# Kernel optimization log

Measured on AMD Instinct MI355X. Metric: run time of the kernel, lower is better.

The kernel has to match this reference:

```python
import jax, jax.numpy as jnp
import numpy as np

EPS = 1e-5

def _sparse_conv(x, nbr, W):
    # x: [N, Cin], nbr: [N, K] indices into rows of x, W: [K, Cin, Cout]
    # Minkowski-style kernel-map conv: gather neighbor feats, contract per offset.
    return jnp.einsum('nkc,kcd->nd', x[nbr], W)

def _bn(x, gamma, beta):
    # BatchNorm over all points (training-mode, biased variance)
    mu = x.mean(axis=0)
    var = x.var(axis=0)
    return (x - mu) * jax.lax.rsqrt(var + EPS) * gamma + beta

def setup_inputs() -> dict:
    key = jax.random.key(0)
    ks = jax.random.split(key, 6)
    N, K, Cin, Cout = 100000, 27, 64, 128
    x = jax.random.normal(ks[0], (N, Cin), dtype=jnp.float32)
    nbr = jax.random.randint(ks[1], (N, K), 0, N, dtype=jnp.int64)
    W1 = jax.random.normal(ks[2], (K, Cin, Cout), dtype=jnp.float32) / np.sqrt(K * Cin)
    W2 = jax.random.normal(ks[3], (K, Cout, Cout), dtype=jnp.float32) / np.sqrt(K * Cout)
    Wd = jax.random.normal(ks[4], (Cin, Cout), dtype=jnp.float32) / np.sqrt(Cin)
    ones = jnp.ones((Cout,), jnp.float32)
    zeros = jnp.zeros((Cout,), jnp.float32)
    return {"x": x, "nbr": nbr, "W1": W1, "g1": ones, "b1": zeros,
            "W2": W2, "g2": ones, "b2": zeros, "Wd": Wd, "gd": ones, "bd": zeros}

def reference(x, nbr, W1, g1, b1, W2, g2, b2, Wd, gd, bd):
    h = jax.nn.relu(_bn(_sparse_conv(x, nbr, W1), g1, b1))
    h = jax.nn.relu(_bn(_sparse_conv(h, nbr, W2), g2, b2))
    # downsample branch (input_nc != output_nc): 1x1 sparse conv == matmul, + BN
    res = _bn(x @ Wd, gd, bd)
    return h + res
```

## Files before the change

kernel.cpp:

```cpp
#include <hip/hip_runtime.h>
#include <hip/hip_bf16.h>

typedef unsigned short u16;
typedef unsigned int   u32;

#define COUT 128
#define KNB  27

typedef __attribute__((ext_vector_type(8))) __bf16 bf16x8;
typedef __attribute__((ext_vector_type(4))) float  f32x4;

__device__ float g_sum[2][128], g_sq[2][128];
__device__ float g_colsum[64], g_G[4096];
__device__ float g_sc[3][128], g_sh[3][128];
__device__ int   g_f32;
__device__ int   g_i64;
__device__ __attribute__((aligned(16))) u16 g_W1t[KNB * 128 * 64];
__device__ __attribute__((aligned(16))) u16 g_W2t[KNB * 128 * 128];

__device__ __forceinline__ float b2f(u32 u) {
    union { float f; u32 i; } v; v.i = u << 16; return v.f;
}
__device__ __forceinline__ u16 f2b(float f) {
    union { float f; u32 i; } v; v.f = f;
    u32 r = v.i + 0x7fffu + ((v.i >> 16) & 1u);
    return (u16)(r >> 16);
}
__device__ __forceinline__ float ldf(const void* p, int i, bool f32) {
    return f32 ? ((const float*)p)[i] : b2f((u32)((const u16*)p)[i]);
}

__device__ __forceinline__ void gld16(const void* g, void* l) {
    __builtin_amdgcn_global_load_lds(
        (const __attribute__((address_space(1))) u32*)g,
        (__attribute__((address_space(3))) u32*)l, 16, 0, 0);
}

__device__ __forceinline__ void lds_sync() {
    asm volatile("s_waitcnt lgkmcnt(0)" ::: "memory");
    __builtin_amdgcn_s_barrier();
    asm volatile("" ::: "memory");
}

__global__ void probe_zero_kernel(const u16* __restrict__ g1w, const int* __restrict__ nbr)
{
    int t = threadIdx.x;
    if (t == 0) {
        g_f32 = (g1w[0] == 0) ? 1 : 0;
        g_i64 = ((nbr[1] | nbr[3] | nbr[5] | nbr[7]) == 0) ? 1 : 0;
    }
    for (int i = t; i < 128; i += 256) {
        g_sum[0][i] = 0.f; g_sq[0][i] = 0.f;
        g_sum[1][i] = 0.f; g_sq[1][i] = 0.f;
    }
    for (int i = t; i < 64; i += 256) g_colsum[i] = 0.f;
    for (int i = t; i < 4096; i += 256) g_G[i] = 0.f;
}

__global__ void convert_w_kernel(const void* __restrict__ W1, const void* __restrict__ W2,
                                 const void* __restrict__ x, u16* __restrict__ xb, int N)
{
    const bool f32 = (g_f32 != 0);
    const int total1 = KNB * 64 * 128;
    const int total2 = KNB * 128 * 128;
    const int stride = gridDim.x * 256;
    for (int e = blockIdx.x * 256 + threadIdx.x; e < total1 + total2; e += stride) {
        if (e < total1) {
            int k = e / (64 * 128), r = e % (64 * 128);
            int c = r / 128, d = r % 128;
            g_W1t[(k * 128 + d) * 64 + c] = f2b(ldf(W1, e, f32));
        } else {
            int e2 = e - total1;
            int k = e2 / (128 * 128), r = e2 % (128 * 128);
            int c = r / 128, d = r % 128;
            g_W2t[(k * 128 + d) * 128 + c] = f2b(ldf(W2, e2, f32));
        }
    }
    const int totalx4 = (N * 64) / 4;
    for (int e = blockIdx.x * 256 + threadIdx.x; e < totalx4; e += stride) {
        if (f32) {
            float4 v = ((const float4*)x)[e];
            ushort4 r;
            r.x = f2b(v.x); r.y = f2b(v.y); r.z = f2b(v.z); r.w = f2b(v.w);
            ((ushort4*)xb)[e] = r;
        } else {
            ((uint2*)xb)[e] = ((const uint2*)x)[e];
        }
    }
}

__global__ __launch_bounds__(256)
void bn_relu_kernel(u16* __restrict__ tmp, int N)
{
    const int t  = threadIdx.x;
    const int c0 = (t & 15) * 8;
    float sc[8], sh[8];
#pragma unroll
    for (int j = 0; j < 8; ++j) { sc[j] = g_sc[0][c0 + j]; sh[j] = g_sh[0][c0 + j]; }
    const int total = N * (COUT / 8);
    for (int e = blockIdx.x * 256 + t; e < total; e += gridDim.x * 256) {
        uint4 u = ((const uint4*)tmp)[e];
        float v[8] = { b2f(u.x & 0xffffu), b2f(u.x >> 16),
                       b2f(u.y & 0xffffu), b2f(u.y >> 16),
                       b2f(u.z & 0xffffu), b2f(u.z >> 16),
                       b2f(u.w & 0xffffu), b2f(u.w >> 16) };
#pragma unroll
        for (int j = 0; j < 8; ++j) v[j] = fmaxf(fmaf(v[j], sc[j], sh[j]), 0.f);
        uint4 o;
        o.x = (u32)f2b(v[0]) | ((u32)f2b(v[1]) << 16);
        o.y = (u32)f2b(v[2]) | ((u32)f2b(v[3]) << 16);
        o.z = (u32)f2b(v[4]) | ((u32)f2b(v[5]) << 16);
        o.w = (u32)f2b(v[6]) | ((u32)f2b(v[7]) << 16);
        ((uint4*)tmp)[e] = o;
    }
}

template<int CIN, bool OUTF32, int WSEL, int SSEL>
__global__ __launch_bounds__(256, 2)
void spconv_mfma(const u16* __restrict__ src, const int* __restrict__ nbr,
                 void* __restrict__ outv, int N)
{
    constexpr int CHUNKS  = CIN / 64;
    constexpr int STEPS   = KNB * CHUNKS;
    constexpr int MAINEND = STEPS & ~1;
    const u16* __restrict__ Wt = (WSEL == 1) ? g_W1t : g_W2t;

    __shared__ __attribute__((aligned(16))) u16 As[2 * 8192];
    __shared__ __attribute__((aligned(16))) u16 Bs[2 * 8192];
    __shared__ u32 nbrl[128 * 28];

    const int t    = threadIdx.x;
    const int lane = t & 63;
    const int w    = t >> 6;
    const int mh   = lane & 15;
    const int qh   = lane >> 4;
    const int wm   = w >> 1;
    const int wn   = w & 1;
    const int n0   = blockIdx.x * 128;
    const int kst  = (g_i64 != 0) ? 2 : 1;

    const int r8   = lane >> 3;
    const int gaw  = ((lane & 7) ^ (r8 & 7)) * 8;

    for (int e = t; e < 128 * KNB; e += 256) {
        int row = e / KNB, kk = e - row * KNB;
        int gr  = n0 + row;
        int grc = (gr < N) ? gr : (N - 1);
        nbrl[row * 28 + kk] = (u32)nbr[(size_t)grc * (KNB * kst) + (size_t)kk * kst];
    }
    __syncthreads();

    int aoff[2][4];
#pragma unroll
    for (int mt = 0; mt < 4; ++mt) {
        int rr   = wm * 64 + mt * 16 + mh;
        int base = (rr >> 3) * 512 + (rr & 7) * 64;
        aoff[0][mt] = base + ((qh       ^ (mh & 7)) * 8);
        aoff[1][mt] = base + (((4 + qh) ^ (mh & 7)) * 8);
    }

    f32x4 acc[4][4];
#pragma unroll
    for (int a = 0; a < 4; ++a)
#pragma unroll
        for (int b = 0; b < 4; ++b) acc[a][b] = (f32x4){0.f, 0.f, 0.f, 0.f};

    int idx0[4], idxE[4], idxO[4];

#define KOF(S)  ((CHUNKS == 2) ? ((S) >> 1) : (S))
#define CB(S)   ((CHUNKS == 2) ? (((S) & 1) * 64) : 0)

#define IDXRD(DST, S) do { \
    int kk_ = KOF(S); if (kk_ > KNB - 1) kk_ = KNB - 1; \
    _Pragma("unroll") \
    for (int j_ = 0; j_ < 4; ++j_) \
        DST[j_] = (int)nbrl[(w * 32 + j_ * 8 + r8) * 28 + kk_]; \
} while (0)

#define ISSUE_STEP(BUFO, IDX, S) do { \
    const int cb_ = CB(S); const int k_ = KOF(S); \
    _Pragma("unroll") \
    for (int j_ = 0; j_ < 4; ++j_) { \
        u32 r_ = (u32)(IDX)[j_]; if (r_ >= (u32)N) r_ = 0; \
        gld16(src + (size_t)r_ * CIN + cb_ + gaw, \
              &As[(BUFO) + (w * 4 + j_) * 512]); \
    } \
    _Pragma("unroll") \
    for (int j_ = 0; j_ < 4; ++j_) { \
        const int sx_ = w * 4 + j_;                     \
        gld16(Wt + ((size_t)k_ * 128 + (sx_ >> 1) * 16 + mh) * CIN + cb_ \
                 + (sx_ & 1) * 32 + qh * 8, \
              &Bs[(BUFO) + sx_ * 512]); \
    } \
} while (0)

#define MFMA_PHASE(BUFO) do { \
    __builtin_amdgcn_s_setprio(1); \
    _Pragma("unroll") \
    for (int ks_ = 0; ks_ < 2; ++ks_) { \
        bf16x8 af_[4]; \
        _Pragma("unroll") \
        for (int mt_ = 0; mt_ < 4; ++mt_) \
            af_[mt_] = *(const bf16x8*)&As[(BUFO) + aoff[ks_][mt_]]; \
        _Pragma("unroll") \
        for (int nt_ = 0; nt_ < 4; ++nt_) { \
            bf16x8 bf_ = *(const bf16x8*)&Bs[(BUFO) + \
                (((wn * 4 + nt_) * 2 + ks_) * 512) + lane * 8]; \
            _Pragma("unroll") \
            for (int mt_ = 0; mt_ < 4; ++mt_) \
                acc[mt_][nt_] = __builtin_amdgcn_mfma_f32_16x16x32_bf16( \
                    af_[mt_], bf_, acc[mt_][nt_], 0, 0, 0); \
        } \
    } \
    __builtin_amdgcn_s_setprio(0); \
} while (0)

    IDXRD(idx0, 0);
    IDXRD(idxO, 1);
    ISSUE_STEP(0, idx0, 0);
    IDXRD(idxE, 2);

#pragma clang loop unroll(disable)
    for (int s = 0; s < MAINEND; s += 2) {
        lds_sync();
        ISSUE_STEP(8192, idxO, s + 1);
        IDXRD(idxO, s + 3);
        asm volatile("s_waitcnt vmcnt(8)" ::: "memory");
        __builtin_amdgcn_s_barrier();
        asm volatile("" ::: "memory");
        MFMA_PHASE(0);

        lds_sync();
        if (s + 2 < STEPS) {
            ISSUE_STEP(0, idxE, s + 2);
            IDXRD(idxE, s + 4);
            asm volatile("s_waitcnt vmcnt(8)" ::: "memory");
        } else {
            asm volatile("s_waitcnt vmcnt(0)" ::: "memory");
        }
        __builtin_amdgcn_s_barrier();
        asm volatile("" ::: "memory");
        MFMA_PHASE(8192);
    }
    if constexpr (STEPS & 1) {
        lds_sync();
        asm volatile("s_waitcnt vmcnt(0)" ::: "memory");
        __builtin_amdgcn_s_barrier();
        asm volatile("" ::: "memory");
        MFMA_PHASE(0);
    }

#pragma unroll
    for (int mt = 0; mt < 4; ++mt) {
#pragma unroll
        for (int r4 = 0; r4 < 4; ++r4) {
            int gr = n0 + (wm * 4 + mt) * 16 + qh * 4 + r4;
            if (gr < N) {
#pragma unroll
                for (int nt = 0; nt < 4; ++nt) {
                    float val = acc[mt][nt][r4];
                    size_t off = (size_t)gr * COUT + (wn * 4 + nt) * 16 + mh;
                    if constexpr (OUTF32) ((float*)outv)[off] = val;
                    else                  ((u16*)outv)[off]   = f2b(val);
                }
            }
        }
    }

    if constexpr (SSEL >= 0) {
        float sS[4], sQ[4];
#pragma unroll
        for (int nt = 0; nt < 4; ++nt) { sS[nt] = 0.f; sQ[nt] = 0.f; }
#pragma unroll
        for (int mt = 0; mt < 4; ++mt) {
#pragma unroll
            for (int r4 = 0; r4 < 4; ++r4) {
                int gr = n0 + (wm * 4 + mt) * 16 + qh * 4 + r4;
                bool ok = (gr < N);
#pragma unroll
                for (int nt = 0; nt < 4; ++nt) {
                    float v = ok ? acc[mt][nt][r4] : 0.f;
                    sS[nt] += v;
                    sQ[nt] = fmaf(v, v, sQ[nt]);
                }
            }
        }
#pragma unroll
        for (int nt = 0; nt < 4; ++nt) {
            sS[nt] += __shfl_xor(sS[nt], 16);
            sS[nt] += __shfl_xor(sS[nt], 32);
            sQ[nt] += __shfl_xor(sQ[nt], 16);
            sQ[nt] += __shfl_xor(sQ[nt], 32);
        }
        lds_sync();
        float* red = (float*)As;
        if (lane < 16) {
#pragma unroll
            for (int nt = 0; nt < 4; ++nt) {
                red[w * 64 + nt * 16 + lane]       = sS[nt];
                red[256 + w * 64 + nt * 16 + lane] = sQ[nt];
            }
        }
        lds_sync();
        if (t < 128) {
            int hi = t >> 6, lo = t & 63;
            float S = red[hi * 64 + lo] + red[(hi + 2) * 64 + lo];
            float Q = red[256 + hi * 64 + lo] + red[256 + (hi + 2) * 64 + lo];
            atomicAdd(&g_sum[SSEL][t], S);
            atomicAdd(&g_sq[SSEL][t],  Q);
        }
    }
#undef KOF
#undef CB
#undef IDXRD
#undef ISSUE_STEP
#undef MFMA_PHASE
}

template<int SEL>
__global__ void finalize_kernel(const void* __restrict__ g, const void* __restrict__ b,
                                float invN)
{
    const bool f32 = (g_f32 != 0);
    int c = threadIdx.x;
    float mu  = g_sum[SEL][c] * invN;
    float var = fmaxf(g_sq[SEL][c] * invN - mu * mu, 0.f);
    float rs  = rsqrtf(var + 1e-5f);
    float sc  = rs * ldf(g, c, f32);
    g_sc[SEL][c] = sc;
    g_sh[SEL][c] = ldf(b, c, f32) - mu * sc;
}

__global__ __launch_bounds__(256)
void xstats_kernel(const void* __restrict__ xv, int N)
{
    __shared__ float xs[16 * 64];
    const bool f32 = (g_f32 != 0);
    const int t  = threadIdx.x;
    const int c  = t >> 2;
    const int cb = (t & 3) * 16;
    float acc[16];
#pragma unroll
    for (int j = 0; j < 16; ++j) acc[j] = 0.f;
    float cs = 0.f;

    for (int r0 = blockIdx.x * 16; r0 < N; r0 += gridDim.x * 16) {
        __syncthreads();
        {
            int e = t * 4;
            int rr = e >> 6, qq = e & 63;
            int row = r0 + rr;
            size_t off = (size_t)min(row, N - 1) * 64 + qq;
            bool ok = (row < N);
            float v0, v1, v2, v3;
            if (f32) {
                float4 vv = *(const float4*)((const float*)xv + off);
                v0 = vv.x; v1 = vv.y; v2 = vv.z; v3 = vv.w;
            } else {
                uint2 u = *(const uint2*)((const u16*)xv + off);
                v0 = b2f(u.x & 0xffffu); v1 = b2f(u.x >> 16);
                v2 = b2f(u.y & 0xffffu); v3 = b2f(u.y >> 16);
            }
            xs[e + 0] = ok ? v0 : 0.f;
            xs[e + 1] = ok ? v1 : 0.f;
            xs[e + 2] = ok ? v2 : 0.f;
            xs[e + 3] = ok ? v3 : 0.f;
        }
        __syncthreads();
#pragma unroll
        for (int rr = 0; rr < 16; ++rr) {
            float a = xs[rr * 64 + c];
#pragma unroll
            for (int j = 0; j < 16; ++j)
                acc[j] = fmaf(a, xs[rr * 64 + cb + j], acc[j]);
        }
        if (t < 64) {
#pragma unroll
            for (int rr = 0; rr < 16; ++rr) cs += xs[rr * 64 + t];
        }
    }
#pragma unroll
    for (int j = 0; j < 16; ++j) atomicAdd(&g_G[c * 64 + cb + j], acc[j]);
    if (t < 64) atomicAdd(&g_colsum[t], cs);
}

__global__ __launch_bounds__(128)
void finalize_d_kernel(const void* __restrict__ Wd, const void* __restrict__ gd,
                       const void* __restrict__ bd, float invN)
{
    __shared__ float Gs[64 * 64];
    const bool f32 = (g_f32 != 0);
    const int t = threadIdx.x;
    for (int e = t; e < 4096; e += 128) Gs[e] = g_G[e];
    __syncthreads();
    float w[64];
#pragma unroll
    for (int c = 0; c < 64; ++c) w[c] = ldf(Wd, c * 128 + t, f32);
    float s = 0.f, q = 0.f;
    for (int c = 0; c < 64; ++c) {
        float inner = 0.f;
#pragma unroll 8
        for (int cc = 0; cc < 64; ++cc) inner = fmaf(Gs[c * 64 + cc], w[cc], inner);
        q = fmaf(w[c], inner, q);
        s = fmaf(g_colsum[c], w[c], s);
    }
    float mu  = s * invN;
    float var = fmaxf(q * invN - mu * mu, 0.f);
    float rs  = rsqrtf(var + 1e-5f);
    float sc  = rs * ldf(gd, t, f32);
    g_sc[2][t] = sc;
    g_sh[2][t] = ldf(bd, t, f32) - mu * sc;
}

__global__ __launch_bounds__(256)
void finish_dense_kernel(const void* __restrict__ xv, const void* __restrict__ Wdv,
                         float* __restrict__ out, int N)
{
    __shared__ float Xs[64 * 68];
    __shared__ float Ws[64 * COUT];
    const bool f32 = (g_f32 != 0);
    const int t  = threadIdx.x;
    const int tx = t & 31;
    const int ty = t >> 5;
    const int n0 = blockIdx.x * 64;
    const int valid = min(64, N - n0);

    for (int e = t; e < 64 * 16; e += 256) {
        int mm = e >> 4;
        int qq = (e & 15) << 2;
        size_t off = (size_t)min(n0 + mm, N - 1) * 64 + qq;
        float v0, v1, v2, v3;
        if (f32) {
            float4 vv = *(const float4*)((const float*)xv + off);
            v0 = vv.x; v1 = vv.y; v2 = vv.z; v3 = vv.w;
        } else {
            uint2 u = *(const uint2*)((const u16*)xv + off);
            v0 = b2f(u.x & 0xffffu); v1 = b2f(u.x >> 16);
            v2 = b2f(u.y & 0xffffu); v3 = b2f(u.y >> 16);
        }
        *(float4*)&Xs[mm * 68 + qq] = make_float4(v0, v1, v2, v3);
    }
    if (f32) {
        const float* Wp = (const float*)Wdv;
        for (int e = t; e < (64 * COUT) / 8; e += 256) {
            int l = e << 3;
            float4 a = *(const float4*)(Wp + l);
            float4 b = *(const float4*)(Wp + l + 4);
            float* dst = &Ws[l];
            dst[0]=a.x; dst[1]=a.y; dst[2]=a.z; dst[3]=a.w;
            dst[4]=b.x; dst[5]=b.y; dst[6]=b.z; dst[7]=b.w;
        }
    } else {
        const u16* Wp = (const u16*)Wdv;
        for (int e = t; e < (64 * COUT) / 8; e += 256) {
            int l = e << 3;
            uint4 u = *(const uint4*)(Wp + l);
            float* dst = &Ws[l];
            dst[0] = b2f(u.x & 0xffffu); dst[1] = b2f(u.x >> 16);
            dst[2] = b2f(u.y & 0xffffu); dst[3] = b2f(u.y >> 16);
            dst[4] = b2f(u.z & 0xffffu); dst[5] = b2f(u.z >> 16);
            dst[6] = b2f(u.w & 0xffffu); dst[7] = b2f(u.w >> 16);
        }
    }
    __syncthreads();

    float acc[8][4];
#pragma unroll
    for (int mm = 0; mm < 8; ++mm)
#pragma unroll
        for (int j = 0; j < 4; ++j) acc[mm][j] = 0.f;

#pragma unroll 2
    for (int c = 0; c < 64; ++c) {
        float4 wv = *(const float4*)&Ws[c * COUT + tx * 4];
#pragma unroll
        for (int mm = 0; mm < 8; ++mm) {
            float a = Xs[(ty * 8 + mm) * 68 + c];
            acc[mm][0] = fmaf(a, wv.x, acc[mm][0]);
            acc[mm][1] = fmaf(a, wv.y, acc[mm][1]);
            acc[mm][2] = fmaf(a, wv.z, acc[mm][2]);
            acc[mm][3] = fmaf(a, wv.w, acc[mm][3]);
        }
    }

    const int d = tx * 4;
    float s2r[4] = {g_sc[1][d], g_sc[1][d+1], g_sc[1][d+2], g_sc[1][d+3]};
    float h2r[4] = {g_sh[1][d], g_sh[1][d+1], g_sh[1][d+2], g_sh[1][d+3]};
    float sdr[4] = {g_sc[2][d], g_sc[2][d+1], g_sc[2][d+2], g_sc[2][d+3]};
    float hdr[4] = {g_sh[2][d], g_sh[2][d+1], g_sh[2][d+2], g_sh[2][d+3]};
#pragma unroll
    for (int mm = 0; mm < 8; ++mm) {
        int rr = ty * 8 + mm;
        if (rr < valid) {
            float* p = out + (size_t)(n0 + rr) * COUT + d;
            float4 raw = *(float4*)p;
            float o0 = fmaxf(fmaf(raw.x, s2r[0], h2r[0]), 0.f) + fmaf(acc[mm][0], sdr[0], hdr[0]);
            float o1 = fmaxf(fmaf(raw.y, s2r[1], h2r[1]), 0.f) + fmaf(acc[mm][1], sdr[1], hdr[1]);
            float o2 = fmaxf(fmaf(raw.z, s2r[2], h2r[2]), 0.f) + fmaf(acc[mm][2], sdr[2], hdr[2]);
            float o3 = fmaxf(fmaf(raw.w, s2r[3], h2r[3]), 0.f) + fmaf(acc[mm][3], sdr[3], hdr[3]);
            *(float4*)p = make_float4(o0, o1, o2, o3);
        }
    }
}

extern "C" void kernel_launch(void* const* d_in, const int* in_sizes, int n_in,
                              void* d_out, int out_size, void* d_ws, size_t ws_size,
                              hipStream_t stream)
{
    const void* x   = d_in[0];
    const int*  nbr = (const int*)d_in[1];
    const void* W1  = d_in[2];
    const void* g1  = d_in[3];
    const void* b1  = d_in[4];
    const void* W2  = d_in[5];
    const void* g2  = d_in[6];
    const void* b2  = d_in[7];
    const void* Wd  = d_in[8];
    const void* gd  = d_in[9];
    const void* bd  = d_in[10];
    float* out = (float*)d_out;

    const int N = in_sizes[0] / 64;
    u16* tmp = (u16*)d_ws;
    u16* xb  = (u16*)d_out;

    const int nbm = (N + 127) / 128;
    const int nbf = (N + 63) / 64;
    const float invN = 1.f / (float)N;

    hipLaunchKernelGGL(probe_zero_kernel, dim3(1), dim3(256), 0, stream,
                       (const u16*)g1, nbr);
    hipLaunchKernelGGL(convert_w_kernel, dim3(1024), dim3(256), 0, stream,
                       W1, W2, x, xb, N);
    hipLaunchKernelGGL((spconv_mfma<64, false, 1, 0>), dim3(nbm), dim3(256), 0, stream,
                       xb, nbr, tmp, N);
    hipLaunchKernelGGL((finalize_kernel<0>), dim3(1), dim3(128), 0, stream, g1, b1, invN);
    hipLaunchKernelGGL(bn_relu_kernel, dim3(2048), dim3(256), 0, stream, tmp, N);
    hipLaunchKernelGGL((spconv_mfma<128, true, 2, 1>), dim3(nbm), dim3(256), 0, stream,
                       tmp, nbr, out, N);
    hipLaunchKernelGGL((finalize_kernel<1>), dim3(1), dim3(128), 0, stream, g2, b2, invN);
    hipLaunchKernelGGL(xstats_kernel, dim3(256), dim3(256), 0, stream, x, N);
    hipLaunchKernelGGL(finalize_d_kernel, dim3(1), dim3(128), 0, stream, Wd, gd, bd, invN);
    hipLaunchKernelGGL(finish_dense_kernel, dim3(nbf), dim3(256), 0, stream,
                       x, Wd, out, N);
}
```

Measured before the change: 704.5 us.

## Triple-buffer gathered A tiles and load neighbor indices directly from global

The sparse-conv MFMA kernel now keeps three LDS buffers for the gathered neighbor-feature tile, so A tiles are prefetched two steps ahead, while weights stay double-buffered one step ahead. The loop is a six-step unrolled region with a deeper vmcnt wait. The up-front staging of the neighbor index table into LDS, and its block-wide barrier, is removed; each thread reads its indices straight from global memory several steps ahead. The aim is to hide gather latency better and drop the prologue, at the cost of more LDS for A, more in-flight loads and registers, and some wasted loads in the trailing regions past the last step.

```diff
diff --git a/kernel.cpp b/kernel.cpp
--- a/kernel.cpp
+++ b/kernel.cpp
@@ -120,14 +120,12 @@
 void spconv_mfma(const u16* __restrict__ src, const int* __restrict__ nbr,
                  void* __restrict__ outv, int N)
 {
-    constexpr int CHUNKS  = CIN / 64;
-    constexpr int STEPS   = KNB * CHUNKS;
-    constexpr int MAINEND = STEPS & ~1;
+    constexpr int CHUNKS = CIN / 64;
+    constexpr int STEPS  = KNB * CHUNKS;
     const u16* __restrict__ Wt = (WSEL == 1) ? g_W1t : g_W2t;
 
-    __shared__ __attribute__((aligned(16))) u16 As[2 * 8192];
+    __shared__ __attribute__((aligned(16))) u16 As[3 * 8192];
     __shared__ __attribute__((aligned(16))) u16 Bs[2 * 8192];
-    __shared__ u32 nbrl[128 * 28];
 
     const int t    = threadIdx.x;
     const int lane = t & 63;
@@ -142,13 +140,13 @@
     const int r8   = lane >> 3;
     const int gaw  = ((lane & 7) ^ (r8 & 7)) * 8;
 
-    for (int e = t; e < 128 * KNB; e += 256) {
-        int row = e / KNB, kk = e - row * KNB;
-        int gr  = n0 + row;
+    u32 nb[4];
+#pragma unroll
+    for (int j = 0; j < 4; ++j) {
+        int gr  = n0 + w * 32 + j * 8 + r8;
         int grc = (gr < N) ? gr : (N - 1);
-        nbrl[row * 28 + kk] = (u32)nbr[(size_t)grc * (KNB * kst) + (size_t)kk * kst];
-    }
-    __syncthreads();
+        nb[j] = (u32)grc * (u32)(KNB * kst);
+    }
 
     int aoff[2][4];
 #pragma unroll
@@ -165,46 +163,51 @@
 #pragma unroll
         for (int b = 0; b < 4; ++b) acc[a][b] = (f32x4){0.f, 0.f, 0.f, 0.f};
 
-    int idx0[4], idxE[4], idxO[4];
-
-#define KOF(S)  ((CHUNKS == 2) ? ((S) >> 1) : (S))
-#define CB(S)   ((CHUNKS == 2) ? (((S) & 1) * 64) : 0)
-
-#define IDXRD(DST, S) do { \
-    int kk_ = KOF(S); if (kk_ > KNB - 1) kk_ = KNB - 1; \
+    int ix[3][4];
+
+#define KOFC(S) ((CHUNKS == 2) ? ((S) >> 1) : (S))
+#define CBC(S)  ((CHUNKS == 2) ? (((S) & 1) * 64) : 0)
+
+#define IDXLD(DST, S) do { \
+    int kk_ = KOFC(S); if (kk_ > KNB - 1) kk_ = KNB - 1; \
     _Pragma("unroll") \
     for (int j_ = 0; j_ < 4; ++j_) \
-        DST[j_] = (int)nbrl[(w * 32 + j_ * 8 + r8) * 28 + kk_]; \
+        DST[j_] = (int)nbr[nb[j_] + (u32)kk_ * (u32)kst]; \
 } while (0)
 
-#define ISSUE_STEP(BUFO, IDX, S) do { \
-    const int cb_ = CB(S); const int k_ = KOF(S); \
+#define ISSUE_A(ABUF, IDX, S) do { \
+    const int cb_ = CBC(S); \
     _Pragma("unroll") \
     for (int j_ = 0; j_ < 4; ++j_) { \
         u32 r_ = (u32)(IDX)[j_]; if (r_ >= (u32)N) r_ = 0; \
         gld16(src + (size_t)r_ * CIN + cb_ + gaw, \
-              &As[(BUFO) + (w * 4 + j_) * 512]); \
+              &As[(ABUF) * 8192 + (w * 4 + j_) * 512]); \
     } \
+} while (0)
+
+#define ISSUE_B(BBUF, S) do { \
+    int kk_ = KOFC(S); if (kk_ > KNB - 1) kk_ = KNB - 1; \
+    const int cb_ = CBC(S); \
     _Pragma("unroll") \
     for (int j_ = 0; j_ < 4; ++j_) { \
         const int sx_ = w * 4 + j_;                     \
-        gld16(Wt + ((size_t)k_ * 128 + (sx_ >> 1) * 16 + mh) * CIN + cb_ \
+        gld16(Wt + ((size_t)kk_ * 128 + (sx_ >> 1) * 16 + mh) * CIN + cb_ \
                  + (sx_ & 1) * 32 + qh * 8, \
-              &Bs[(BUFO) + sx_ * 512]); \
+              &Bs[(BBUF) * 8192 + sx_ * 512]); \
     } \
 } while (0)
 
-#define MFMA_PHASE(BUFO) do { \
+#define MFMA_PHASE(ABUF, BBUF) do { \
     __builtin_amdgcn_s_setprio(1); \
     _Pragma("unroll") \
     for (int ks_ = 0; ks_ < 2; ++ks_) { \
         bf16x8 af_[4]; \
         _Pragma("unroll") \
         for (int mt_ = 0; mt_ < 4; ++mt_) \
-            af_[mt_] = *(const bf16x8*)&As[(BUFO) + aoff[ks_][mt_]]; \
+            af_[mt_] = *(const bf16x8*)&As[(ABUF) * 8192 + aoff[ks_][mt_]]; \
         _Pragma("unroll") \
         for (int nt_ = 0; nt_ < 4; ++nt_) { \
-            bf16x8 bf_ = *(const bf16x8*)&Bs[(BUFO) + \
+            bf16x8 bf_ = *(const bf16x8*)&Bs[(BBUF) * 8192 + \
                 (((wn * 4 + nt_) * 2 + ks_) * 512) + lane * 8]; \
             _Pragma("unroll") \
             for (int mt_ = 0; mt_ < 4; ++mt_) \
@@ -215,40 +218,36 @@
     __builtin_amdgcn_s_setprio(0); \
 } while (0)
 
-    IDXRD(idx0, 0);
-    IDXRD(idxO, 1);
-    ISSUE_STEP(0, idx0, 0);
-    IDXRD(idxE, 2);
+#define FENCE() asm volatile("" ::: "memory")
+
+#define REGION(I, SBASE) do { \
+    const int s_ = (SBASE) + (I); \
+    lds_sync(); \
+    ISSUE_B((I + 1) & 1, s_ + 1);                 FENCE(); \
+    ISSUE_A((I + 2) % 3, ix[(I + 2) % 3], s_ + 2); FENCE(); \
+    IDXLD(ix[(I + 1) % 3], s_ + 4); \
+    asm volatile("s_waitcnt vmcnt(20)" ::: "memory"); \
+    __builtin_amdgcn_s_barrier(); \
+    FENCE(); \
+    if (s_ < STEPS) MFMA_PHASE(I % 3, I & 1); \
+} while (0)
+
+    IDXLD(ix[0], 0);
+    IDXLD(ix[1], 1);
+    IDXLD(ix[2], 2);
+    ISSUE_B(0, 0);            FENCE();
+    ISSUE_A(0, ix[0], 0);     FENCE();
+    ISSUE_A(1, ix[1], 1);     FENCE();
+    IDXLD(ix[0], 3);
 
 #pragma clang loop unroll(disable)
-    for (int s = 0; s < MAINEND; s += 2) {
-        lds_sync();
-        ISSUE_STEP(8192, idxO, s + 1);
-        IDXRD(idxO, s + 3);
-        asm volatile("s_waitcnt vmcnt(8)" ::: "memory");
-        __builtin_amdgcn_s_barrier();
-        asm volatile("" ::: "memory");
-        MFMA_PHASE(0);
-
-        lds_sync();
-        if (s + 2 < STEPS) {
-            ISSUE_STEP(0, idxE, s + 2);
-            IDXRD(idxE, s + 4);
-            asm volatile("s_waitcnt vmcnt(8)" ::: "memory");
-        } else {
-            asm volatile("s_waitcnt vmcnt(0)" ::: "memory");
-        }
-        __builtin_amdgcn_s_barrier();
-        asm volatile("" ::: "memory");
-        MFMA_PHASE(8192);
-    }
-    if constexpr (STEPS & 1) {
-        lds_sync();
-        asm volatile("s_waitcnt vmcnt(0)" ::: "memory");
-        __builtin_amdgcn_s_barrier();
-        asm volatile("" ::: "memory");
-        MFMA_PHASE(0);
-    }
+    for (int s = 0; s < STEPS; s += 6) {
+        REGION(0, s); REGION(1, s); REGION(2, s);
+        REGION(3, s); REGION(4, s); REGION(5, s);
+    }
+    asm volatile("s_waitcnt vmcnt(0)" ::: "memory");
+    __builtin_amdgcn_s_barrier();
+    FENCE();
 
 #pragma unroll
     for (int mt = 0; mt < 4; ++mt) {
@@ -310,11 +309,14 @@
             atomicAdd(&g_sq[SSEL][t],  Q);
         }
     }
-#undef KOF
-#undef CB
-#undef IDXRD
-#undef ISSUE_STEP
+#undef KOFC
+#undef CBC
+#undef IDXLD
+#undef ISSUE_A
+#undef ISSUE_B
 #undef MFMA_PHASE
+#undef FENCE
+#undef REGION
 }
 
 template<int SEL>
```

Result: no change. 718.3 us (+2.0%).

## Split first conv gather into row-range passes and fuse x-stats and finalize kernels

Applied to the files above, without the earlier changes.

The first sparse conv now makes four passes over all 27 offsets. Each pass gathers only neighbor rows inside one quarter of the point range and substitutes a zero row for the rest, so each pass's working set of gathered features is smaller and more likely to stay in L2. In exchange, MFMA work and weight loads for that conv grow fourfold. The Gram and column-sum statistics for the downsample branch now run as extra blocks of the conversion kernel, and the BN2 finalize is merged into the downsample finalize kernel, which cuts kernel launches.

```diff
diff --git a/kernel.cpp b/kernel.cpp
--- a/kernel.cpp
+++ b/kernel.cpp
@@ -3,6 +3,7 @@
 
 typedef unsigned short u16;
 typedef unsigned int   u32;
+typedef unsigned long long u64;
 
 #define COUT 128
 #define KNB  27
@@ -15,6 +16,7 @@
 __device__ float g_sc[3][128], g_sh[3][128];
 __device__ int   g_f32;
 __device__ int   g_i64;
+__device__ __attribute__((aligned(128))) u16 g_zero[128];
 __device__ __attribute__((aligned(16))) u16 g_W1t[KNB * 128 * 64];
 __device__ __attribute__((aligned(16))) u16 g_W2t[KNB * 128 * 128];
 
@@ -57,36 +59,91 @@
     for (int i = t; i < 4096; i += 256) g_G[i] = 0.f;
 }
 
-__global__ void convert_w_kernel(const void* __restrict__ W1, const void* __restrict__ W2,
-                                 const void* __restrict__ x, u16* __restrict__ xb, int N)
+__global__ __launch_bounds__(256)
+void convert_w_kernel(const void* __restrict__ W1, const void* __restrict__ W2,
+                      const void* __restrict__ x, u16* __restrict__ xb, int N)
 {
     const bool f32 = (g_f32 != 0);
-    const int total1 = KNB * 64 * 128;
-    const int total2 = KNB * 128 * 128;
-    const int stride = gridDim.x * 256;
-    for (int e = blockIdx.x * 256 + threadIdx.x; e < total1 + total2; e += stride) {
-        if (e < total1) {
-            int k = e / (64 * 128), r = e % (64 * 128);
-            int c = r / 128, d = r % 128;
-            g_W1t[(k * 128 + d) * 64 + c] = f2b(ldf(W1, e, f32));
-        } else {
-            int e2 = e - total1;
-            int k = e2 / (128 * 128), r = e2 % (128 * 128);
-            int c = r / 128, d = r % 128;
-            g_W2t[(k * 128 + d) * 128 + c] = f2b(ldf(W2, e2, f32));
-        }
-    }
-    const int totalx4 = (N * 64) / 4;
-    for (int e = blockIdx.x * 256 + threadIdx.x; e < totalx4; e += stride) {
-        if (f32) {
-            float4 v = ((const float4*)x)[e];
-            ushort4 r;
-            r.x = f2b(v.x); r.y = f2b(v.y); r.z = f2b(v.z); r.w = f2b(v.w);
-            ((ushort4*)xb)[e] = r;
-        } else {
-            ((uint2*)xb)[e] = ((const uint2*)x)[e];
-        }
-    }
+    const int bid = blockIdx.x;
+    const int t   = threadIdx.x;
+    __shared__ float xs[16 * 64];
+
+    if (bid < 1024) {
+        const int total1 = KNB * 64 * 128;
+        const int total2 = KNB * 128 * 128;
+        const int stride = 1024 * 256;
+        for (int e = bid * 256 + t; e < total1 + total2; e += stride) {
+            if (e < total1) {
+                int k = e / (64 * 128), r = e % (64 * 128);
+                int c = r / 128, d = r % 128;
+                g_W1t[(k * 128 + d) * 64 + c] = f2b(ldf(W1, e, f32));
+            } else {
+                int e2 = e - total1;
+                int k = e2 / (128 * 128), r = e2 % (128 * 128);
+                int c = r / 128, d = r % 128;
+                g_W2t[(k * 128 + d) * 128 + c] = f2b(ldf(W2, e2, f32));
+            }
+        }
+        const int totalx4 = (N * 64) / 4;
+        for (int e = bid * 256 + t; e < totalx4; e += stride) {
+            if (f32) {
+                float4 v = ((const float4*)x)[e];
+                ushort4 r;
+                r.x = f2b(v.x); r.y = f2b(v.y); r.z = f2b(v.z); r.w = f2b(v.w);
+                ((ushort4*)xb)[e] = r;
+            } else {
+                ((uint2*)xb)[e] = ((const uint2*)x)[e];
+            }
+        }
+        return;
+    }
+
+    const int b2 = bid - 1024;
+    const int c  = t >> 2;
+    const int cb = (t & 3) * 16;
+    float acc[16];
+#pragma unroll
+    for (int j = 0; j < 16; ++j) acc[j] = 0.f;
+    float cs = 0.f;
+
+    for (int r0 = b2 * 16; r0 < N; r0 += 256 * 16) {
+        __syncthreads();
+        {
+            int e = t * 4;
+            int rr = e >> 6, qq = e & 63;
+            int row = r0 + rr;
+            size_t off = (size_t)min(row, N - 1) * 64 + qq;
+            bool ok = (row < N);
+            float v0, v1, v2, v3;
+            if (f32) {
+                float4 vv = *(const float4*)((const float*)x + off);
+                v0 = vv.x; v1 = vv.y; v2 = vv.z; v3 = vv.w;
+            } else {
+                uint2 u = *(const uint2*)((const u16*)x + off);
+                v0 = b2f(u.x & 0xffffu); v1 = b2f(u.x >> 16);
+                v2 = b2f(u.y & 0xffffu); v3 = b2f(u.y >> 16);
+            }
+            xs[e + 0] = ok ? v0 : 0.f;
+            xs[e + 1] = ok ? v1 : 0.f;
+            xs[e + 2] = ok ? v2 : 0.f;
+            xs[e + 3] = ok ? v3 : 0.f;
+        }
+        __syncthreads();
+#pragma unroll
+        for (int rr = 0; rr < 16; ++rr) {
+            float a = xs[rr * 64 + c];
+#pragma unroll
+            for (int j = 0; j < 16; ++j)
+                acc[j] = fmaf(a, xs[rr * 64 + cb + j], acc[j]);
+        }
+        if (t < 64) {
+#pragma unroll
+            for (int rr = 0; rr < 16; ++rr) cs += xs[rr * 64 + t];
+        }
+    }
+#pragma unroll
+    for (int j = 0; j < 16; ++j) atomicAdd(&g_G[c * 64 + cb + j], acc[j]);
+    if (t < 64) atomicAdd(&g_colsum[t], cs);
 }
 
 __global__ __launch_bounds__(256)
@@ -115,14 +172,14 @@
     }
 }
 
-template<int CIN, bool OUTF32, int WSEL, int SSEL>
+template<int CIN, int PASSES, bool OUTF32, int WSEL, int SSEL>
 __global__ __launch_bounds__(256, 2)
 void spconv_mfma(const u16* __restrict__ src, const int* __restrict__ nbr,
                  void* __restrict__ outv, int N)
 {
-    constexpr int CHUNKS  = CIN / 64;
-    constexpr int STEPS   = KNB * CHUNKS;
-    constexpr int MAINEND = STEPS & ~1;
+    constexpr int CHUNKS = CIN / 64;
+    constexpr int PERK   = KNB * CHUNKS;
+    constexpr int ST     = PASSES * PERK;
     const u16* __restrict__ Wt = (WSEL == 1) ? g_W1t : g_W2t;
 
     __shared__ __attribute__((aligned(16))) u16 As[2 * 8192];
@@ -167,23 +224,36 @@
 
     int idx0[4], idxE[4], idxO[4];
 
-#define KOF(S)  ((CHUNKS == 2) ? ((S) >> 1) : (S))
-#define CB(S)   ((CHUNKS == 2) ? (((S) & 1) * 64) : 0)
+#define KOF(S)  ((CHUNKS == 2) ? (((S) % PERK) >> 1) : ((S) % PERK))
+#define CBOF(S) ((CHUNKS == 2) ? ((((S) % PERK) & 1) * 64) : 0)
 
 #define IDXRD(DST, S) do { \
-    int kk_ = KOF(S); if (kk_ > KNB - 1) kk_ = KNB - 1; \
+    int kk_ = KOF(S); \
     _Pragma("unroll") \
     for (int j_ = 0; j_ < 4; ++j_) \
         DST[j_] = (int)nbrl[(w * 32 + j_ * 8 + r8) * 28 + kk_]; \
 } while (0)
 
 #define ISSUE_STEP(BUFO, IDX, S) do { \
-    const int cb_ = CB(S); const int k_ = KOF(S); \
+    const int cb_ = CBOF(S); const int k_ = KOF(S); \
+    u32 lo_ = 0, hi_ = (u32)N; \
+    if constexpr (PASSES > 1) { \
+        const u32 p_ = (u32)((S) / PERK); \
+        lo_ = (u32)(((u64)p_ * (u32)N) / PASSES); \
+        hi_ = (u32)(((u64)(p_ + 1) * (u32)N) / PASSES); \
+    } \
     _Pragma("unroll") \
     for (int j_ = 0; j_ < 4; ++j_) { \
         u32 r_ = (u32)(IDX)[j_]; if (r_ >= (u32)N) r_ = 0; \
-        gld16(src + (size_t)r_ * CIN + cb_ + gaw, \
-              &As[(BUFO) + (w * 4 + j_) * 512]); \
+        const u16* sp_; \
+        if constexpr (PASSES > 1) { \
+            bool in_ = (r_ - lo_) < (hi_ - lo_); \
+            sp_ = in_ ? (src + (size_t)r_ * CIN + cb_ + gaw) \
+                      : ((const u16*)g_zero + gaw); \
+        } else { \
+            sp_ = src + (size_t)r_ * CIN + cb_ + gaw; \
+        } \
+        gld16(sp_, &As[(BUFO) + (w * 4 + j_) * 512]); \
     } \
     _Pragma("unroll") \
     for (int j_ = 0; j_ < 4; ++j_) { \
@@ -221,7 +291,7 @@
     IDXRD(idxE, 2);
 
 #pragma clang loop unroll(disable)
-    for (int s = 0; s < MAINEND; s += 2) {
+    for (int s = 0; s < ST; s += 2) {
         lds_sync();
         ISSUE_STEP(8192, idxO, s + 1);
         IDXRD(idxO, s + 3);
@@ -231,7 +301,7 @@
         MFMA_PHASE(0);
 
         lds_sync();
-        if (s + 2 < STEPS) {
+        if (s + 2 < ST) {
             ISSUE_STEP(0, idxE, s + 2);
             IDXRD(idxE, s + 4);
             asm volatile("s_waitcnt vmcnt(8)" ::: "memory");
@@ -241,13 +311,6 @@
         __builtin_amdgcn_s_barrier();
         asm volatile("" ::: "memory");
         MFMA_PHASE(8192);
-    }
-    if constexpr (STEPS & 1) {
-        lds_sync();
-        asm volatile("s_waitcnt vmcnt(0)" ::: "memory");
-        __builtin_amdgcn_s_barrier();
-        asm volatile("" ::: "memory");
-        MFMA_PHASE(0);
     }
 
 #pragma unroll
@@ -311,7 +374,7 @@
         }
     }
 #undef KOF
-#undef CB
+#undef CBOF
 #undef IDXRD
 #undef ISSUE_STEP
 #undef MFMA_PHASE
@@ -331,66 +394,24 @@
     g_sh[SEL][c] = ldf(b, c, f32) - mu * sc;
 }
 
-__global__ __launch_bounds__(256)
-void xstats_kernel(const void* __restrict__ xv, int N)
-{
-    __shared__ float xs[16 * 64];
-    const bool f32 = (g_f32 != 0);
-    const int t  = threadIdx.x;
-    const int c  = t >> 2;
-    const int cb = (t & 3) * 16;
-    float acc[16];
-#pragma unroll
-    for (int j = 0; j < 16; ++j) acc[j] = 0.f;
-    float cs = 0.f;
-
-    for (int r0 = blockIdx.x * 16; r0 < N; r0 += gridDim.x * 16) {
-        __syncthreads();
-        {
-            int e = t * 4;
-            int rr = e >> 6, qq = e & 63;
-            int row = r0 + rr;
-            size_t off = (size_t)min(row, N - 1) * 64 + qq;
-            bool ok = (row < N);
-            float v0, v1, v2, v3;
-            if (f32) {
-                float4 vv = *(const float4*)((const float*)xv + off);
-                v0 = vv.x; v1 = vv.y; v2 = vv.z; v3 = vv.w;
-            } else {
-                uint2 u = *(const uint2*)((const u16*)xv + off);
-                v0 = b2f(u.x & 0xffffu); v1 = b2f(u.x >> 16);
-                v2 = b2f(u.y & 0xffffu); v3 = b2f(u.y >> 16);
-            }
-            xs[e + 0] = ok ? v0 : 0.f;
-            xs[e + 1] = ok ? v1 : 0.f;
-            xs[e + 2] = ok ? v2 : 0.f;
-            xs[e + 3] = ok ? v3 : 0.f;
-        }
-        __syncthreads();
-#pragma unroll
-        for (int rr = 0; rr < 16; ++rr) {
-            float a = xs[rr * 64 + c];
-#pragma unroll
-            for (int j = 0; j < 16; ++j)
-                acc[j] = fmaf(a, xs[rr * 64 + cb + j], acc[j]);
-        }
-        if (t < 64) {
-#pragma unroll
-            for (int rr = 0; rr < 16; ++rr) cs += xs[rr * 64 + t];
-        }
-    }
-#pragma unroll
-    for (int j = 0; j < 16; ++j) atomicAdd(&g_G[c * 64 + cb + j], acc[j]);
-    if (t < 64) atomicAdd(&g_colsum[t], cs);
-}
-
 __global__ __launch_bounds__(128)
-void finalize_d_kernel(const void* __restrict__ Wd, const void* __restrict__ gd,
-                       const void* __restrict__ bd, float invN)
+void finalize2_kernel(const void* __restrict__ g2, const void* __restrict__ b2,
+                      const void* __restrict__ Wd, const void* __restrict__ gd,
+                      const void* __restrict__ bd, float invN)
 {
     __shared__ float Gs[64 * 64];
     const bool f32 = (g_f32 != 0);
     const int t = threadIdx.x;
+
+    {
+        float mu  = g_sum[1][t] * invN;
+        float var = fmaxf(g_sq[1][t] * invN - mu * mu, 0.f);
+        float rs  = rsqrtf(var + 1e-5f);
+        float sc  = rs * ldf(g2, t, f32);
+        g_sc[1][t] = sc;
+        g_sh[1][t] = ldf(b2, t, f32) - mu * sc;
+    }
+
     for (int e = t; e < 4096; e += 128) Gs[e] = g_G[e];
     __syncthreads();
     float w[64];
@@ -530,17 +551,16 @@
 
     hipLaunchKernelGGL(probe_zero_kernel, dim3(1), dim3(256), 0, stream,
                        (const u16*)g1, nbr);
-    hipLaunchKernelGGL(convert_w_kernel, dim3(1024), dim3(256), 0, stream,
+    hipLaunchKernelGGL(convert_w_kernel, dim3(1280), dim3(256), 0, stream,
                        W1, W2, x, xb, N);
-    hipLaunchKernelGGL((spconv_mfma<64, false, 1, 0>), dim3(nbm), dim3(256), 0, stream,
+    hipLaunchKernelGGL((spconv_mfma<64, 4, false, 1, 0>), dim3(nbm), dim3(256), 0, stream,
                        xb, nbr, tmp, N);
     hipLaunchKernelGGL((finalize_kernel<0>), dim3(1), dim3(128), 0, stream, g1, b1, invN);
     hipLaunchKernelGGL(bn_relu_kernel, dim3(2048), dim3(256), 0, stream, tmp, N);
-    hipLaunchKernelGGL((spconv_mfma<128, true, 2, 1>), dim3(nbm), dim3(256), 0, stream,
+    hipLaunchKernelGGL((spconv_mfma<128, 1, true, 2, 1>), dim3(nbm), dim3(256), 0, stream,
                        tmp, nbr, out, N);
-    hipLaunchKernelGGL((finalize_kernel<1>), dim3(1), dim3(128), 0, stream, g2, b2, invN);
-    hipLaunchKernelGGL(xstats_kernel, dim3(256), dim3(256), 0, stream, x, N);
-    hipLaunchKernelGGL(finalize_d_kernel, dim3(1), dim3(128), 0, stream, Wd, gd, bd, invN);
+    hipLaunchKernelGGL(finalize2_kernel, dim3(1), dim3(128), 0, stream,
+                       g2, b2, Wd, gd, bd, invN);
     hipLaunchKernelGGL(finish_dense_kernel, dim3(nbf), dim3(256), 0, stream,
                        x, Wd, out, N);
 }
```

New measurement: 901.7 us. 1.28x slower.

## Fold BN finalize and x-stats kernels into neighboring kernels to cut launches

Applied to the files above, without the earlier changes.

Removes the three finalize kernels and the separate xstats kernel. Per-channel BN scale and shift are now recomputed inline in bn_relu and finish_dense, and the downsample-branch stats come from extra blocks added to the weight-convert kernel. Block 0 of the second sparse conv finalizes the downsample BN before its main work. The weight-transpose loop is also reordered so that writes are contiguous. This cuts launch and serialization overhead but adds redundant per-block finalize work, and it makes one conv block do a serial 64x64 reduction. That reduction reads g_G and g_colsum, which must be complete from the earlier convert launch; stream ordering guarantees this.

```diff
diff --git a/kernel.cpp b/kernel.cpp
--- a/kernel.cpp
+++ b/kernel.cpp
@@ -12,7 +12,7 @@
 
 __device__ float g_sum[2][128], g_sq[2][128];
 __device__ float g_colsum[64], g_G[4096];
-__device__ float g_sc[3][128], g_sh[3][128];
+__device__ float g_scd[128], g_shd[128];
 __device__ int   g_f32;
 __device__ int   g_i64;
 __device__ __attribute__((aligned(16))) u16 g_W1t[KNB * 128 * 64];
@@ -57,46 +57,111 @@
     for (int i = t; i < 4096; i += 256) g_G[i] = 0.f;
 }
 
-__global__ void convert_w_kernel(const void* __restrict__ W1, const void* __restrict__ W2,
-                                 const void* __restrict__ x, u16* __restrict__ xb, int N)
+__global__ __launch_bounds__(256)
+void convert_w_kernel(const void* __restrict__ W1, const void* __restrict__ W2,
+                      const void* __restrict__ x, u16* __restrict__ xb, int N)
 {
     const bool f32 = (g_f32 != 0);
-    const int total1 = KNB * 64 * 128;
-    const int total2 = KNB * 128 * 128;
-    const int stride = gridDim.x * 256;
-    for (int e = blockIdx.x * 256 + threadIdx.x; e < total1 + total2; e += stride) {
-        if (e < total1) {
-            int k = e / (64 * 128), r = e % (64 * 128);
-            int c = r / 128, d = r % 128;
-            g_W1t[(k * 128 + d) * 64 + c] = f2b(ldf(W1, e, f32));
-        } else {
-            int e2 = e - total1;
-            int k = e2 / (128 * 128), r = e2 % (128 * 128);
-            int c = r / 128, d = r % 128;
-            g_W2t[(k * 128 + d) * 128 + c] = f2b(ldf(W2, e2, f32));
-        }
-    }
-    const int totalx4 = (N * 64) / 4;
-    for (int e = blockIdx.x * 256 + threadIdx.x; e < totalx4; e += stride) {
-        if (f32) {
-            float4 v = ((const float4*)x)[e];
-            ushort4 r;
-            r.x = f2b(v.x); r.y = f2b(v.y); r.z = f2b(v.z); r.w = f2b(v.w);
-            ((ushort4*)xb)[e] = r;
-        } else {
-            ((uint2*)xb)[e] = ((const uint2*)x)[e];
-        }
-    }
+    const int bid = blockIdx.x;
+    const int t   = threadIdx.x;
+    __shared__ float xs[16 * 64];
+
+    if (bid < 1024) {
+        const int total1 = KNB * 128 * 64;
+        const int total2 = KNB * 128 * 128;
+        const int stride = 1024 * 256;
+        for (int e = bid * 256 + t; e < total1 + total2; e += stride) {
+            if (e < total1) {
+                int k = e / (128 * 64), r = e % (128 * 64);
+                int d = r >> 6, c = r & 63;
+                g_W1t[e] = f2b(ldf(W1, (k * 64 + c) * 128 + d, f32));
+            } else {
+                int e2 = e - total1;
+                int k = e2 / (128 * 128), r = e2 % (128 * 128);
+                int d = r >> 7, c = r & 127;
+                g_W2t[e2] = f2b(ldf(W2, (k * 128 + c) * 128 + d, f32));
+            }
+        }
+        const int totalx4 = (N * 64) / 4;
+        for (int e = bid * 256 + t; e < totalx4; e += stride) {
+            if (f32) {
+                float4 v = ((const float4*)x)[e];
+                ushort4 r;
+                r.x = f2b(v.x); r.y = f2b(v.y); r.z = f2b(v.z); r.w = f2b(v.w);
+                ((ushort4*)xb)[e] = r;
+            } else {
+                ((uint2*)xb)[e] = ((const uint2*)x)[e];
+            }
+        }
+        return;
+    }
+
+    const int b2 = bid - 1024;
+    const int c  = t >> 2;
+    const int cb = (t & 3) * 16;
+    float acc[16];
+#pragma unroll
+    for (int j = 0; j < 16; ++j) acc[j] = 0.f;
+    float cs = 0.f;
+
+    for (int r0 = b2 * 16; r0 < N; r0 += 256 * 16) {
+        __syncthreads();
+        {
+            int e = t * 4;
+            int rr = e >> 6, qq = e & 63;
+            int row = r0 + rr;
+            size_t off = (size_t)min(row, N - 1) * 64 + qq;
+            bool ok = (row < N);
+            float v0, v1, v2, v3;
+            if (f32) {
+                float4 vv = *(const float4*)((const float*)x + off);
+                v0 = vv.x; v1 = vv.y; v2 = vv.z; v3 = vv.w;
+            } else {
+                uint2 u = *(const uint2*)((const u16*)x + off);
+                v0 = b2f(u.x & 0xffffu); v1 = b2f(u.x >> 16);
+                v2 = b2f(u.y & 0xffffu); v3 = b2f(u.y >> 16);
+            }
+            xs[e + 0] = ok ? v0 : 0.f;
+            xs[e + 1] = ok ? v1 : 0.f;
+            xs[e + 2] = ok ? v2 : 0.f;
+            xs[e + 3] = ok ? v3 : 0.f;
+        }
+        __syncthreads();
+#pragma unroll
+        for (int rr = 0; rr < 16; ++rr) {
+            float a = xs[rr * 64 + c];
+#pragma unroll
+            for (int j = 0; j < 16; ++j)
+                acc[j] = fmaf(a, xs[rr * 64 + cb + j], acc[j]);
+        }
+        if (t < 64) {
+#pragma unroll
+            for (int rr = 0; rr < 16; ++rr) cs += xs[rr * 64 + t];
+        }
+    }
+#pragma unroll
+    for (int j = 0; j < 16; ++j) atomicAdd(&g_G[c * 64 + cb + j], acc[j]);
+    if (t < 64) atomicAdd(&g_colsum[t], cs);
 }
 
 __global__ __launch_bounds__(256)
-void bn_relu_kernel(u16* __restrict__ tmp, int N)
+void bn_relu_kernel(u16* __restrict__ tmp, const void* __restrict__ g1,
+                    const void* __restrict__ b1, float invN, int N)
 {
+    const bool f32 = (g_f32 != 0);
     const int t  = threadIdx.x;
     const int c0 = (t & 15) * 8;
     float sc[8], sh[8];
 #pragma unroll
-    for (int j = 0; j < 8; ++j) { sc[j] = g_sc[0][c0 + j]; sh[j] = g_sh[0][c0 + j]; }
+    for (int j = 0; j < 8; ++j) {
+        int c = c0 + j;
+        float mu  = g_sum[0][c] * invN;
+        float var = fmaxf(g_sq[0][c] * invN - mu * mu, 0.f);
+        float rs  = rsqrtf(var + 1e-5f);
+        float s   = rs * ldf(g1, c, f32);
+        sc[j] = s;
+        sh[j] = ldf(b1, c, f32) - mu * s;
+    }
     const int total = N * (COUT / 8);
     for (int e = blockIdx.x * 256 + t; e < total; e += gridDim.x * 256) {
         uint4 u = ((const uint4*)tmp)[e];
@@ -115,10 +180,12 @@
     }
 }
 
-template<int CIN, bool OUTF32, int WSEL, int SSEL>
+template<int CIN, bool OUTF32, int WSEL, int SSEL, bool BND>
 __global__ __launch_bounds__(256, 2)
 void spconv_mfma(const u16* __restrict__ src, const int* __restrict__ nbr,
-                 void* __restrict__ outv, int N)
+                 void* __restrict__ outv, int N,
+                 const void* __restrict__ Wd, const void* __restrict__ gd,
+                 const void* __restrict__ bd, float invN)
 {
     constexpr int CHUNKS  = CIN / 64;
     constexpr int STEPS   = KNB * CHUNKS;
@@ -138,6 +205,28 @@
     const int wn   = w & 1;
     const int n0   = blockIdx.x * 128;
     const int kst  = (g_i64 != 0) ? 2 : 1;
+
+    if constexpr (BND) {
+        if (blockIdx.x == 0 && t < 128) {
+            const bool f32 = (g_f32 != 0);
+            float s = 0.f, q = 0.f;
+            for (int c = 0; c < 64; ++c) {
+                float wc = ldf(Wd, c * 128 + t, f32);
+                float inner = 0.f;
+#pragma unroll 8
+                for (int cc = 0; cc < 64; ++cc)
+                    inner = fmaf(g_G[c * 64 + cc], ldf(Wd, cc * 128 + t, f32), inner);
+                q = fmaf(wc, inner, q);
+                s = fmaf(g_colsum[c], wc, s);
+            }
+            float mu  = s * invN;
+            float var = fmaxf(q * invN - mu * mu, 0.f);
+            float rs  = rsqrtf(var + 1e-5f);
+            float sc  = rs * ldf(gd, t, f32);
+            g_scd[t] = sc;
+            g_shd[t] = ldf(bd, t, f32) - mu * sc;
+        }
+    }
 
     const int r8   = lane >> 3;
     const int gaw  = ((lane & 7) ^ (r8 & 7)) * 8;
@@ -317,104 +406,10 @@
 #undef MFMA_PHASE
 }
 
-template<int SEL>
-__global__ void finalize_kernel(const void* __restrict__ g, const void* __restrict__ b,
-                                float invN)
-{
-    const bool f32 = (g_f32 != 0);
-    int c = threadIdx.x;
-    float mu  = g_sum[SEL][c] * invN;
-    float var = fmaxf(g_sq[SEL][c] * invN - mu * mu, 0.f);
-    float rs  = rsqrtf(var + 1e-5f);
-    float sc  = rs * ldf(g, c, f32);
-    g_sc[SEL][c] = sc;
-    g_sh[SEL][c] = ldf(b, c, f32) - mu * sc;
-}
-
-__global__ __launch_bounds__(256)
-void xstats_kernel(const void* __restrict__ xv, int N)
-{
-    __shared__ float xs[16 * 64];
-    const bool f32 = (g_f32 != 0);
-    const int t  = threadIdx.x;
-    const int c  = t >> 2;
-    const int cb = (t & 3) * 16;
-    float acc[16];
-#pragma unroll
-    for (int j = 0; j < 16; ++j) acc[j] = 0.f;
-    float cs = 0.f;
-
-    for (int r0 = blockIdx.x * 16; r0 < N; r0 += gridDim.x * 16) {
-        __syncthreads();
-        {
-            int e = t * 4;
-            int rr = e >> 6, qq = e & 63;
-            int row = r0 + rr;
-            size_t off = (size_t)min(row, N - 1) * 64 + qq;
-            bool ok = (row < N);
-            float v0, v1, v2, v3;
-            if (f32) {
-                float4 vv = *(const float4*)((const float*)xv + off);
-                v0 = vv.x; v1 = vv.y; v2 = vv.z; v3 = vv.w;
-            } else {
-                uint2 u = *(const uint2*)((const u16*)xv + off);
-                v0 = b2f(u.x & 0xffffu); v1 = b2f(u.x >> 16);
-                v2 = b2f(u.y & 0xffffu); v3 = b2f(u.y >> 16);
-            }
-            xs[e + 0] = ok ? v0 : 0.f;
-            xs[e + 1] = ok ? v1 : 0.f;
-            xs[e + 2] = ok ? v2 : 0.f;
-            xs[e + 3] = ok ? v3 : 0.f;
-        }
-        __syncthreads();
-#pragma unroll
-        for (int rr = 0; rr < 16; ++rr) {
-            float a = xs[rr * 64 + c];
-#pragma unroll
-            for (int j = 0; j < 16; ++j)
-                acc[j] = fmaf(a, xs[rr * 64 + cb + j], acc[j]);
-        }
-        if (t < 64) {
-#pragma unroll
-            for (int rr = 0; rr < 16; ++rr) cs += xs[rr * 64 + t];
-        }
-    }
-#pragma unroll
-    for (int j = 0; j < 16; ++j) atomicAdd(&g_G[c * 64 + cb + j], acc[j]);
-    if (t < 64) atomicAdd(&g_colsum[t], cs);
-}
-
-__global__ __launch_bounds__(128)
-void finalize_d_kernel(const void* __restrict__ Wd, const void* __restrict__ gd,
-                       const void* __restrict__ bd, float invN)
-{
-    __shared__ float Gs[64 * 64];
-    const bool f32 = (g_f32 != 0);
-    const int t = threadIdx.x;
-    for (int e = t; e < 4096; e += 128) Gs[e] = g_G[e];
-    __syncthreads();
-    float w[64];
-#pragma unroll
-    for (int c = 0; c < 64; ++c) w[c] = ldf(Wd, c * 128 + t, f32);
-    float s = 0.f, q = 0.f;
-    for (int c = 0; c < 64; ++c) {
-        float inner = 0.f;
-#pragma unroll 8
-        for (int cc = 0; cc < 64; ++cc) inner = fmaf(Gs[c * 64 + cc], w[cc], inner);
-        q = fmaf(w[c], inner, q);
-        s = fmaf(g_colsum[c], w[c], s);
-    }
-    float mu  = s * invN;
-    float var = fmaxf(q * invN - mu * mu, 0.f);
-    float rs  = rsqrtf(var + 1e-5f);
-    float sc  = rs * ldf(gd, t, f32);
-    g_sc[2][t] = sc;
-    g_sh[2][t] = ldf(bd, t, f32) - mu * sc;
-}
-
 __global__ __launch_bounds__(256)
 void finish_dense_kernel(const void* __restrict__ xv, const void* __restrict__ Wdv,
-                         float* __restrict__ out, int N)
+                         const void* __restrict__ g2, const void* __restrict__ b2,
+                         float invN, float* __restrict__ out, int N)
 {
     __shared__ float Xs[64 * 68];
     __shared__ float Ws[64 * COUT];
@@ -484,10 +479,18 @@
     }
 
     const int d = tx * 4;
-    float s2r[4] = {g_sc[1][d], g_sc[1][d+1], g_sc[1][d+2], g_sc[1][d+3]};
-    float h2r[4] = {g_sh[1][d], g_sh[1][d+1], g_sh[1][d+2], g_sh[1][d+3]};
-    float sdr[4] = {g_sc[2][d], g_sc[2][d+1], g_sc[2][d+2], g_sc[2][d+3]};
-    float hdr[4] = {g_sh[2][d], g_sh[2][d+1], g_sh[2][d+2], g_sh[2][d+3]};
+    float s2r[4], h2r[4];
+#pragma unroll
+    for (int j = 0; j < 4; ++j) {
+        float mu  = g_sum[1][d + j] * invN;
+        float var = fmaxf(g_sq[1][d + j] * invN - mu * mu, 0.f);
+        float rs  = rsqrtf(var + 1e-5f);
+        float s   = rs * ldf(g2, d + j, f32);
+        s2r[j] = s;
+        h2r[j] = ldf(b2, d + j, f32) - mu * s;
+    }
+    float sdr[4] = {g_scd[d], g_scd[d+1], g_scd[d+2], g_scd[d+3]};
+    float hdr[4] = {g_shd[d], g_shd[d+1], g_shd[d+2], g_shd[d+3]};
 #pragma unroll
     for (int mm = 0; mm < 8; ++mm) {
         int rr = ty * 8 + mm;
@@ -530,17 +533,14 @@
 
     hipLaunchKernelGGL(probe_zero_kernel, dim3(1), dim3(256), 0, stream,
                        (const u16*)g1, nbr);
-    hipLaunchKernelGGL(convert_w_kernel, dim3(1024), dim3(256), 0, stream,
+    hipLaunchKernelGGL(convert_w_kernel, dim3(1280), dim3(256), 0, stream,
                        W1, W2, x, xb, N);
-    hipLaunchKernelGGL((spconv_mfma<64, false, 1, 0>), dim3(nbm), dim3(256), 0, stream,
-                       xb, nbr, tmp, N);
-    hipLaunchKernelGGL((finalize_kernel<0>), dim3(1), dim3(128), 0, stream, g1, b1, invN);
-    hipLaunchKernelGGL(bn_relu_kernel, dim3(2048), dim3(256), 0, stream, tmp, N);
-    hipLaunchKernelGGL((spconv_mfma<128, true, 2, 1>), dim3(nbm), dim3(256), 0, stream,
-                       tmp, nbr, out, N);
-    hipLaunchKernelGGL((finalize_kernel<1>), dim3(1), dim3(128), 0, stream, g2, b2, invN);
-    hipLaunchKernelGGL(xstats_kernel, dim3(256), dim3(256), 0, stream, x, N);
-    hipLaunchKernelGGL(finalize_d_kernel, dim3(1), dim3(128), 0, stream, Wd, gd, bd, invN);
+    hipLaunchKernelGGL((spconv_mfma<64, false, 1, 0, false>), dim3(nbm), dim3(256), 0,
+                       stream, xb, nbr, tmp, N, nullptr, nullptr, nullptr, 0.f);
+    hipLaunchKernelGGL(bn_relu_kernel, dim3(2048), dim3(256), 0, stream,
+                       tmp, g1, b1, invN, N);
+    hipLaunchKernelGGL((spconv_mfma<128, true, 2, 1, true>), dim3(nbm), dim3(256), 0,
+                       stream, tmp, nbr, out, N, Wd, gd, bd, invN);
     hipLaunchKernelGGL(finish_dense_kernel, dim3(nbf), dim3(256), 0, stream,
-                       x, Wd, out, N);
-}
+                       x, Wd, g2, b2, invN, out, N);
+}
```

New measurement: 761.8 us. 1.08x slower.
